# Optimization experiments

Hardware: AMD Instinct MI355X
Metric: run time of the kernel (lower is better)

## Reference

```python
import jax, jax.numpy as jnp
import numpy as np


def setup_inputs() -> dict:
    key = jax.random.key(0)
    k1, k2 = jax.random.split(key)
    x = jax.random.normal(k1, (128, 25, 512), dtype=jnp.float32)
    high = jax.random.normal(k2, (64, 20, 512), dtype=jnp.float32)  # (C, n, d)
    return {"x": x, "high": high}


def reference(x, high):
    # x: (b, res, d); high: (C, n, d) learned per-class support basis
    b, res, d = x.shape
    C, n, _ = high.shape
    q = x.reshape(b * res, d)                     # (Q, d)
    lam = n / d                                   # ridge coefficient = n/d
    ct = jnp.swapaxes(high, 1, 2)                 # (C, d, n)
    cct = high @ ct                               # (C, n, n) small Gram matrices
    inv = jnp.linalg.inv(cct + lam * jnp.eye(n, dtype=x.dtype))  # (C, n, n)
    ctinv = ct @ inv @ high                       # (C, d, d) per-class projector
    # reconstruct each query through each class projector: (C, Q, d)
    t = jnp.einsum('qd,cde->cqe', q, ctinv)
    dist = jnp.sum((t - q[None, :, :]) ** 2, axis=2).T  # (Q, C)
    logits = -dist.reshape(b, res, C).mean(axis=1)       # (b, C)
    # min-max scaler per row
    mn = logits.min(axis=1, keepdims=True)
    mx = logits.max(axis=1, keepdims=True)
    return (logits - mn) / (mx - mn)
```

## Files before the change

kernel.cpp:

```cpp
#include <hip/hip_runtime.h>

typedef __bf16 v8bf __attribute__((ext_vector_type(8)));
typedef float  v4f  __attribute__((ext_vector_type(4)));

#define D     512
#define NSUP  20
#define NC    64
#define RES   25
#define BB    128
#define LAM   (20.0f/512.0f)
#define KT    32
#define NKT   (D/KT)
#define CPB   8
#define COLS  160

__device__ __forceinline__ ushort bf_hi(float v) {
    uint32_t b = __float_as_uint(v);
    return (ushort)((b + 0x7FFF + ((b >> 16) & 1)) >> 16);
}
__device__ __forceinline__ float us2f(ushort u) {
    return __uint_as_float(((uint32_t)u) << 16);
}

__global__ __launch_bounds__(256) void k_prep(const float* __restrict__ high,
                                              ushort* __restrict__ Hth,
                                              ushort* __restrict__ Htl) {
    const int cls  = blockIdx.x;
    const int half = blockIdx.y;
    const int t    = threadIdx.x;
    __shared__ float Hc[NSUP * 516];
    __shared__ float Gs[NSUP * NSUP];
    __shared__ float Ls[400], Rs[400], rL[NSUP];

    for (int i = t; i < NSUP * (D / 4); i += 256) {
        int r = i >> 7, c4 = (i & 127) << 2;
        *(float4*)&Hc[r * 516 + c4] = *(const float4*)&high[(cls * NSUP + r) * D + c4];
    }
    __syncthreads();

    for (int e = t; e < NSUP * NSUP; e += 256) {
        int i = e / NSUP, j = e % NSUP;
        if (i <= j) {
            float s = 0.f;
            for (int k = 0; k < D; k += 4) {
                float4 a = *(float4*)&Hc[i * 516 + k];
                float4 b = *(float4*)&Hc[j * 516 + k];
                s += a.x * b.x + a.y * b.y + a.z * b.z + a.w * b.w;
            }
            Gs[i * NSUP + j] = s;
            Gs[j * NSUP + i] = s;
        }
    }
    __syncthreads();

    if (t < 64) {
        const int c  = t & 31;
        const int gp = t >> 5;
        const float dlam = gp ? 2.0f * LAM : LAM;
        float m[NSUP];
        if (c < NSUP) {
            #pragma unroll
            for (int i = 0; i < NSUP; ++i) m[i] = Gs[i * NSUP + c];
            #pragma unroll
            for (int i = 0; i < NSUP; ++i) if (i == c) m[i] += dlam;
        }
        #pragma unroll
        for (int k = 0; k < NSUP; ++k) {
            float piv = __shfl(m[k], k, 32);
            float sq  = sqrtf(piv);
            float rsq = 1.0f / sq;
            float lck = m[k] * rsq;
            if (c == k) {
                m[k] = sq;
                #pragma unroll
                for (int i = k + 1; i < NSUP; ++i) m[i] *= rsq;
            }
            #pragma unroll
            for (int i = k + 1; i < NSUP; ++i) {
                float lik = __shfl(m[i], k, 32);
                if (c > k) m[i] -= lik * lck;
            }
        }
        if (c < NSUP) {
            float* Lout = gp ? Rs : Ls;
            #pragma unroll
            for (int i = 0; i < NSUP; ++i) if (i >= c) Lout[i * NSUP + c] = m[i];
            if (!gp) rL[c] = 1.0f / m[c];
        }
    }
    __syncthreads();

    const int col = half * 256 + t;
    float h[NSUP];
    #pragma unroll
    for (int m = 0; m < NSUP; ++m) h[m] = Hc[m * 516 + col];
    #pragma unroll
    for (int i = 0; i < NSUP; ++i) {
        float s = h[i];
        #pragma unroll
        for (int m = 0; m < i; ++m) s -= Ls[i * NSUP + m] * h[m];
        h[i] = s * rL[i];
    }
    #pragma unroll
    for (int i = NSUP - 1; i >= 0; --i) {
        float s = h[i];
        #pragma unroll
        for (int m = i + 1; m < NSUP; ++m) s -= Ls[m * NSUP + i] * h[m];
        h[i] = s * rL[i];
    }
    #pragma unroll
    for (int i = 0; i < NSUP; ++i) {
        float s = 0.f;
        #pragma unroll
        for (int m = i; m < NSUP; ++m) s += Rs[m * NSUP + i] * h[m];
        ushort hh = bf_hi(s);
        float  rr = s - us2f(hh);
        Hth[(cls * NSUP + i) * D + col] = hh;
        Htl[(cls * NSUP + i) * D + col] = bf_hi(rr);
    }
}

__global__ __launch_bounds__(256, 4) void k_main(const float* __restrict__ x,
                                                 const ushort* __restrict__ Hth,
                                                 const ushort* __restrict__ Htl,
                                                 float* __restrict__ S) {
    const int cg = blockIdx.x, bp = blockIdx.y;
    const int t = threadIdx.x, lane = t & 63, wid = t >> 6;
    const int wm = wid >> 1, wn = wid & 1;
    const int r16 = lane & 15, q = lane >> 4;

    __shared__ float colsum[2][COLS];

    v4f acc[2][5];
    #pragma unroll
    for (int a = 0; a < 2; ++a)
        #pragma unroll
        for (int b = 0; b < 5; ++b) acc[a][b] = (v4f){0.f, 0.f, 0.f, 0.f};

    bool  avalid[2];
    const float* aptr[2];
    #pragma unroll
    for (int mf = 0; mf < 2; ++mf) {
        int f  = wm * 2 + mf;
        int tr = f * 16 + r16;
        int batch = (bp << 1) + (tr >> 5);
        int rb = tr & 31;
        avalid[mf] = rb < RES;
        aptr[mf] = &x[(batch * RES + (avalid[mf] ? rb : 0)) * D + (q << 3)];
    }
    const ushort* bptrh[5];
    const ushort* bptrl[5];
    #pragma unroll
    for (int nf = 0; nf < 5; ++nf) {
        int f   = wn * 5 + nf;
        int row = cg * COLS + f * 16 + r16;
        bptrh[nf] = &Hth[row * D + (q << 3)];
        bptrl[nf] = &Htl[row * D + (q << 3)];
    }

    for (int kt = 0; kt < D; kt += KT) {
        v8bf ah[2], al[2];
        #pragma unroll
        for (int mf = 0; mf < 2; ++mf) {
            float4 v0 = make_float4(0.f, 0.f, 0.f, 0.f), v1 = v0;
            if (avalid[mf]) {
                v0 = *(const float4*)(aptr[mf] + kt);
                v1 = *(const float4*)(aptr[mf] + kt + 4);
            }
            float vv[8] = {v0.x, v0.y, v0.z, v0.w, v1.x, v1.y, v1.z, v1.w};
            #pragma unroll
            for (int e = 0; e < 8; ++e) {
                ushort h = bf_hi(vv[e]);
                float  r = vv[e] - us2f(h);
                ((ushort*)&ah[mf])[e] = h;
                ((ushort*)&al[mf])[e] = bf_hi(r);
            }
        }
        #pragma unroll
        for (int nf = 0; nf < 5; ++nf) {
            v8bf bh = *(const v8bf*)(bptrh[nf] + kt);
            v8bf bl = *(const v8bf*)(bptrl[nf] + kt);
            #pragma unroll
            for (int mf = 0; mf < 2; ++mf) {
                acc[mf][nf] = __builtin_amdgcn_mfma_f32_16x16x32_bf16(ah[mf], bh, acc[mf][nf], 0, 0, 0);
                acc[mf][nf] = __builtin_amdgcn_mfma_f32_16x16x32_bf16(ah[mf], bl, acc[mf][nf], 0, 0, 0);
                acc[mf][nf] = __builtin_amdgcn_mfma_f32_16x16x32_bf16(al[mf], bh, acc[mf][nf], 0, 0, 0);
            }
        }
    }

    #pragma unroll
    for (int nf = 0; nf < 5; ++nf) {
        float part = 0.f;
        #pragma unroll
        for (int mf = 0; mf < 2; ++mf)
            #pragma unroll
            for (int j = 0; j < 4; ++j) part += acc[mf][nf][j] * acc[mf][nf][j];
        part += __shfl_xor(part, 16);
        part += __shfl_xor(part, 32);
        if (q == 0) colsum[wm][wn * 80 + nf * 16 + r16] = part;
    }
    __syncthreads();
    if (t < 16) {
        int b = t >> 3, c = t & 7;
        float s = 0.f;
        #pragma unroll
        for (int i = 0; i < NSUP; ++i) s += colsum[b][c * 20 + i];
        S[((bp << 1) + b) * NC + cg * CPB + c] = s;
    }
}

__global__ __launch_bounds__(64) void k_minmax(const float* __restrict__ S,
                                               float* __restrict__ out) {
    const int b    = blockIdx.x;
    const int lane = threadIdx.x;
    float s  = S[b * NC + lane];
    float mn = s, mx = s;
    #pragma unroll
    for (int off = 32; off > 0; off >>= 1) {
        mn = fminf(mn, __shfl_xor(mn, off, 64));
        mx = fmaxf(mx, __shfl_xor(mx, off, 64));
    }
    out[b * NC + lane] = (s - mn) / (mx - mn);
}

extern "C" void kernel_launch(void* const* d_in, const int* in_sizes, int n_in,
                              void* d_out, int out_size, void* d_ws, size_t ws_size,
                              hipStream_t stream) {
    const float* x    = (const float*)d_in[0];
    const float* high = (const float*)d_in[1];
    float* out = (float*)d_out;

    ushort* Hth = (ushort*)d_ws;
    ushort* Htl = Hth + NC * NSUP * D;
    float*  S   = (float*)(Htl + NC * NSUP * D);

    k_prep  <<<dim3(NC, 2), 256, 0, stream>>>(high, Hth, Htl);
    k_main  <<<dim3(CPB, BB / 2), 256, 0, stream>>>(x, Hth, Htl, S);
    k_minmax<<<BB, 64, 0, stream>>>(S, out);
}
```

Measured before the change: 124.5 us.

## Pre-split x into bf16 hi/lo fragment layout and halve main-kernel tile per block

The fp32-to-bf16 hi/lo split of x moves out of the main GEMM loop into extra blocks of the prep kernel. Both x and the projected support basis are written in an MFMA-fragment-contiguous layout, so each lane does one coalesced 16-byte load per operand per k-step. The main kernel now handles one batch per block instead of two, doubling the grid, and raises the launch-bounds occupancy hint. In exchange it adds a workspace round trip for the split x and gives each block less reuse of the B fragments.

```diff
diff --git a/kernel.cpp b/kernel.cpp
--- a/kernel.cpp
+++ b/kernel.cpp
@@ -13,6 +13,7 @@
 #define NKT   (D/KT)
 #define CPB   8
 #define COLS  160
+#define FRAGSZ (16*D)
 
 __device__ __forceinline__ ushort bf_hi(float v) {
     uint32_t b = __float_as_uint(v);
@@ -21,13 +22,43 @@
 __device__ __forceinline__ float us2f(ushort u) {
     return __uint_as_float(((uint32_t)u) << 16);
 }
+__device__ __forceinline__ int fl_addr(int R, int k) {
+    return (R >> 4) * FRAGSZ + (k >> 3) * 128 + (R & 15) * 8 + (k & 7);
+}
 
 __global__ __launch_bounds__(256) void k_prep(const float* __restrict__ high,
+                                              const float* __restrict__ x,
                                               ushort* __restrict__ Hth,
-                                              ushort* __restrict__ Htl) {
-    const int cls  = blockIdx.x;
-    const int half = blockIdx.y;
-    const int t    = threadIdx.x;
+                                              ushort* __restrict__ Htl,
+                                              ushort* __restrict__ Xh,
+                                              ushort* __restrict__ Xl) {
+    const int t = threadIdx.x;
+
+    if (blockIdx.x >= 128) {
+        const int batch = blockIdx.x - 128;
+        for (int idx = t; idx < 32 * 64; idx += 256) {
+            int r = idx >> 6, o = idx & 63;
+            v8bf hv = (v8bf)(__bf16)0.f, lv = hv;
+            if (r < RES) {
+                const float* p = &x[(batch * RES + r) * D + (o << 3)];
+                float4 v0 = *(const float4*)p, v1 = *(const float4*)(p + 4);
+                float vv[8] = {v0.x, v0.y, v0.z, v0.w, v1.x, v1.y, v1.z, v1.w};
+                #pragma unroll
+                for (int e = 0; e < 8; ++e) {
+                    ushort h = bf_hi(vv[e]);
+                    ((ushort*)&hv)[e] = h;
+                    ((ushort*)&lv)[e] = bf_hi(vv[e] - us2f(h));
+                }
+            }
+            int a = fl_addr(batch * 32 + r, o << 3);
+            *(v8bf*)&Xh[a] = hv;
+            *(v8bf*)&Xl[a] = lv;
+        }
+        return;
+    }
+
+    const int cls  = blockIdx.x >> 1;
+    const int half = blockIdx.x & 1;
     __shared__ float Hc[NSUP * 516];
     __shared__ float Gs[NSUP * NSUP];
     __shared__ float Ls[400], Rs[400], rL[NSUP];
@@ -115,77 +146,51 @@
         for (int m = i; m < NSUP; ++m) s += Rs[m * NSUP + i] * h[m];
         ushort hh = bf_hi(s);
         float  rr = s - us2f(hh);
-        Hth[(cls * NSUP + i) * D + col] = hh;
-        Htl[(cls * NSUP + i) * D + col] = bf_hi(rr);
-    }
-}
-
-__global__ __launch_bounds__(256, 4) void k_main(const float* __restrict__ x,
+        int a = fl_addr(cls * NSUP + i, col);
+        Hth[a] = hh;
+        Htl[a] = bf_hi(rr);
+    }
+}
+
+__global__ __launch_bounds__(256, 8) void k_main(const ushort* __restrict__ Xh,
+                                                 const ushort* __restrict__ Xl,
                                                  const ushort* __restrict__ Hth,
                                                  const ushort* __restrict__ Htl,
                                                  float* __restrict__ S) {
-    const int cg = blockIdx.x, bp = blockIdx.y;
+    const int cg = blockIdx.x, batch = blockIdx.y;
     const int t = threadIdx.x, lane = t & 63, wid = t >> 6;
     const int wm = wid >> 1, wn = wid & 1;
     const int r16 = lane & 15, q = lane >> 4;
 
     __shared__ float colsum[2][COLS];
 
-    v4f acc[2][5];
-    #pragma unroll
-    for (int a = 0; a < 2; ++a)
-        #pragma unroll
-        for (int b = 0; b < 5; ++b) acc[a][b] = (v4f){0.f, 0.f, 0.f, 0.f};
-
-    bool  avalid[2];
-    const float* aptr[2];
-    #pragma unroll
-    for (int mf = 0; mf < 2; ++mf) {
-        int f  = wm * 2 + mf;
-        int tr = f * 16 + r16;
-        int batch = (bp << 1) + (tr >> 5);
-        int rb = tr & 31;
-        avalid[mf] = rb < RES;
-        aptr[mf] = &x[(batch * RES + (avalid[mf] ? rb : 0)) * D + (q << 3)];
-    }
-    const ushort* bptrh[5];
-    const ushort* bptrl[5];
+    v4f acc[5];
+    #pragma unroll
+    for (int b = 0; b < 5; ++b) acc[b] = (v4f){0.f, 0.f, 0.f, 0.f};
+
+    const int abase = (batch * 2 + wm) * FRAGSZ + lane * 8;
+    const ushort* ah_p = Xh + abase;
+    const ushort* al_p = Xl + abase;
+    const ushort* bh_p[5];
+    const ushort* bl_p[5];
     #pragma unroll
     for (int nf = 0; nf < 5; ++nf) {
-        int f   = wn * 5 + nf;
-        int row = cg * COLS + f * 16 + r16;
-        bptrh[nf] = &Hth[row * D + (q << 3)];
-        bptrl[nf] = &Htl[row * D + (q << 3)];
-    }
-
-    for (int kt = 0; kt < D; kt += KT) {
-        v8bf ah[2], al[2];
-        #pragma unroll
-        for (int mf = 0; mf < 2; ++mf) {
-            float4 v0 = make_float4(0.f, 0.f, 0.f, 0.f), v1 = v0;
-            if (avalid[mf]) {
-                v0 = *(const float4*)(aptr[mf] + kt);
-                v1 = *(const float4*)(aptr[mf] + kt + 4);
-            }
-            float vv[8] = {v0.x, v0.y, v0.z, v0.w, v1.x, v1.y, v1.z, v1.w};
-            #pragma unroll
-            for (int e = 0; e < 8; ++e) {
-                ushort h = bf_hi(vv[e]);
-                float  r = vv[e] - us2f(h);
-                ((ushort*)&ah[mf])[e] = h;
-                ((ushort*)&al[mf])[e] = bf_hi(r);
-            }
-        }
+        int fb = (cg * 10 + wn * 5 + nf) * FRAGSZ + lane * 8;
+        bh_p[nf] = Hth + fb;
+        bl_p[nf] = Htl + fb;
+    }
+
+    for (int s = 0; s < NKT; ++s) {
+        const int off = s * 512;
+        v8bf ah = *(const v8bf*)(ah_p + off);
+        v8bf al = *(const v8bf*)(al_p + off);
         #pragma unroll
         for (int nf = 0; nf < 5; ++nf) {
-            v8bf bh = *(const v8bf*)(bptrh[nf] + kt);
-            v8bf bl = *(const v8bf*)(bptrl[nf] + kt);
-            #pragma unroll
-            for (int mf = 0; mf < 2; ++mf) {
-                acc[mf][nf] = __builtin_amdgcn_mfma_f32_16x16x32_bf16(ah[mf], bh, acc[mf][nf], 0, 0, 0);
-                acc[mf][nf] = __builtin_amdgcn_mfma_f32_16x16x32_bf16(ah[mf], bl, acc[mf][nf], 0, 0, 0);
-                acc[mf][nf] = __builtin_amdgcn_mfma_f32_16x16x32_bf16(al[mf], bh, acc[mf][nf], 0, 0, 0);
-            }
+            v8bf bh = *(const v8bf*)(bh_p[nf] + off);
+            v8bf bl = *(const v8bf*)(bl_p[nf] + off);
+            acc[nf] = __builtin_amdgcn_mfma_f32_16x16x32_bf16(ah, bh, acc[nf], 0, 0, 0);
+            acc[nf] = __builtin_amdgcn_mfma_f32_16x16x32_bf16(ah, bl, acc[nf], 0, 0, 0);
+            acc[nf] = __builtin_amdgcn_mfma_f32_16x16x32_bf16(al, bh, acc[nf], 0, 0, 0);
         }
     }
 
@@ -193,20 +198,18 @@
     for (int nf = 0; nf < 5; ++nf) {
         float part = 0.f;
         #pragma unroll
-        for (int mf = 0; mf < 2; ++mf)
-            #pragma unroll
-            for (int j = 0; j < 4; ++j) part += acc[mf][nf][j] * acc[mf][nf][j];
+        for (int j = 0; j < 4; ++j) part += acc[nf][j] * acc[nf][j];
         part += __shfl_xor(part, 16);
         part += __shfl_xor(part, 32);
         if (q == 0) colsum[wm][wn * 80 + nf * 16 + r16] = part;
     }
     __syncthreads();
-    if (t < 16) {
-        int b = t >> 3, c = t & 7;
+    if (t < CPB) {
         float s = 0.f;
         #pragma unroll
-        for (int i = 0; i < NSUP; ++i) s += colsum[b][c * 20 + i];
-        S[((bp << 1) + b) * NC + cg * CPB + c] = s;
+        for (int i = 0; i < NSUP; ++i)
+            s += colsum[0][t * 20 + i] + colsum[1][t * 20 + i];
+        S[batch * NC + cg * CPB + t] = s;
     }
 }
 
@@ -232,10 +235,12 @@
     float* out = (float*)d_out;
 
     ushort* Hth = (ushort*)d_ws;
-    ushort* Htl = Hth + NC * NSUP * D;
-    float*  S   = (float*)(Htl + NC * NSUP * D);
-
-    k_prep  <<<dim3(NC, 2), 256, 0, stream>>>(high, Hth, Htl);
-    k_main  <<<dim3(CPB, BB / 2), 256, 0, stream>>>(x, Hth, Htl, S);
+    ushort* Htl = Hth + 80 * FRAGSZ;
+    ushort* Xh  = Htl + 80 * FRAGSZ;
+    ushort* Xl  = Xh + 256 * FRAGSZ;
+    float*  S   = (float*)(Xl + 256 * FRAGSZ);
+
+    k_prep  <<<256, 256, 0, stream>>>(high, x, Hth, Htl, Xh, Xl);
+    k_main  <<<dim3(CPB, BB), 256, 0, stream>>>(Xh, Xl, Hth, Htl, S);
     k_minmax<<<BB, 64, 0, stream>>>(S, out);
 }
```

Result: slower. 139.1 us (+11.7%).
